# Optimization experiments

Hardware: AMD Instinct MI355X
Metric: run time of the kernel (lower is better)

## Reference

```python
import jax, jax.numpy as jnp
import numpy as np

B, S, D, H = 8, 1024, 1024, 16
DH = D // H  # 64


def setup_inputs() -> dict:
    key0 = jax.random.key(0)
    ks = jax.random.split(key0, 12)
    mk = lambda k, shape: jax.random.normal(k, shape, dtype=jnp.float32)
    inp = {
        "key": mk(ks[0], (B, S, D)),
        "value": mk(ks[1], (B, S, D)),
        "query": mk(ks[2], (B, S, D)),
        "mask": jax.random.randint(ks[3], (B, S, S), 0, 2).astype(jnp.bool_),
        "Wq": mk(ks[4], (D, D)) * 0.02, "bq": jnp.zeros((D,), jnp.float32),
        "Wk": mk(ks[5], (D, D)) * 0.02, "bk": jnp.zeros((D,), jnp.float32),
        "Wv": mk(ks[6], (D, D)) * 0.02, "bv": jnp.zeros((D,), jnp.float32),
        "Wo": mk(ks[7], (D, D)) * 0.02, "bo": jnp.zeros((D,), jnp.float32),
    }
    return inp


def _split_heads(x):
    # [B, S, D] -> [B, H, S, DH]
    return x.reshape(B, -1, H, DH).transpose(0, 2, 1, 3)


def reference(key, value, query, mask, Wq, bq, Wk, bk, Wv, bv, Wo, bo):
    # linear projections (nn.Linear: x @ W.T + b)
    q = _split_heads(query @ Wq.T + bq) / jnp.sqrt(jnp.float32(DH))
    k = _split_heads(key @ Wk.T + bk)
    v = _split_heads(value @ Wv.T + bv)
    # scores: [B, H, Q, K]
    scores = jnp.einsum("bhqd,bhkd->bhqk", q, k)
    scores = jnp.where(mask[:, None, :, :], jnp.float32(-1e18), scores)
    attn = jax.nn.softmax(scores, axis=-1)
    # dropout is identity in eval mode (deterministic reference)
    ctx = jnp.einsum("bhqk,bhkd->bhqd", attn, v)
    ctx = ctx.transpose(0, 2, 1, 3).reshape(B, -1, D)
    out = ctx @ Wo.T + bo
    return out, attn
```

## Files before the change

kernel.cpp:

```cpp
#include <hip/hip_runtime.h>
#include <hip/hip_bf16.h>

#define BB 8
#define SS 1024
#define DD 1024
#define HH 16
#define DHH 64
#define MM (BB*SS)

typedef __attribute__((ext_vector_type(8))) short short8;
typedef __attribute__((ext_vector_type(4))) float f32x4;
typedef __fp16 half2v __attribute__((ext_vector_type(2)));
typedef __fp16 half8 __attribute__((ext_vector_type(8)));

__device__ __forceinline__ unsigned short f2bf(float f) {
  union { __hip_bfloat16 b; unsigned short u; } cv;
  cv.b = __float2bfloat16(f);
  return cv.u;
}
__device__ __forceinline__ float bf2f(unsigned short u) {
  return __builtin_bit_cast(float, (unsigned)u << 16);
}

__global__ void k_conv_w(const float* __restrict__ in, unsigned short* __restrict__ out,
                         float scale, int n8) {
  int i = blockIdx.x * blockDim.x + threadIdx.x;
  if (i >= n8) return;
  const float4* in4 = (const float4*)in;
  float4 a = in4[i * 2];
  float4 b = in4[i * 2 + 1];
  unsigned int w[4];
  w[0] = f2bf(a.x * scale) | ((unsigned)f2bf(a.y * scale) << 16);
  w[1] = f2bf(a.z * scale) | ((unsigned)f2bf(a.w * scale) << 16);
  w[2] = f2bf(b.x * scale) | ((unsigned)f2bf(b.y * scale) << 16);
  w[3] = f2bf(b.z * scale) | ((unsigned)f2bf(b.w * scale) << 16);
  *(uint4*)(out + (size_t)i * 8) = *(uint4*)w;
}

__global__ void k_detect_mask(const unsigned int* __restrict__ m, int* __restrict__ flag) {
  if (threadIdx.x || blockIdx.x) return;
  int i32 = 1, f32m = 1;
  for (int i = 0; i < 64; ++i) {
    unsigned v = m[i];
    if (v > 1u) i32 = 0;
    if (v != 0u && v != 0x3F800000u) f32m = 0;
  }
  *flag = i32 ? 0 : (f32m ? 1 : 2);
}

__global__ void k_maskbits(const void* __restrict__ mask, const int* __restrict__ mmode,
                           unsigned short* __restrict__ out) {
  int i = blockIdx.x * blockDim.x + threadIdx.x;
  if (i >= BB * 32 * 64 * 32) return;
  int r = i & 31, cb = (i >> 5) & 63, qb = (i >> 11) & 31, b = i >> 16;
  size_t src = ((size_t)(b * SS + qb * 32 + r) * SS) + cb * 16;
  int mm = *mmode;
  unsigned short bits = 0;
  if (mm == 2) {
    const unsigned char* p = (const unsigned char*)mask + src;
    uint4 v = *(const uint4*)p;
    const unsigned char* bytes = (const unsigned char*)&v;
#pragma unroll
    for (int c = 0; c < 16; c++) bits |= (bytes[c] ? 1u : 0u) << c;
  } else {
    const unsigned int* p = (const unsigned int*)mask + src;
#pragma unroll
    for (int q = 0; q < 4; q++) {
      uint4 v = *(const uint4*)(p + q * 4);
      bits |= (v.x ? 1u : 0u) << (q * 4 + 0);
      bits |= (v.y ? 1u : 0u) << (q * 4 + 1);
      bits |= (v.z ? 1u : 0u) << (q * 4 + 2);
      bits |= (v.w ? 1u : 0u) << (q * 4 + 3);
    }
  }
  out[i] = bits;
}

__global__ void __launch_bounds__(256, 2) k_gemm_qkv(
    const float* __restrict__ Xq, const float* __restrict__ Xk, const float* __restrict__ Xv,
    const unsigned short* __restrict__ Wqb, const unsigned short* __restrict__ Wkb,
    const unsigned short* __restrict__ Wvb,
    const float* __restrict__ bq, const float* __restrict__ bk, const float* __restrict__ bv,
    unsigned short* __restrict__ Oq, unsigned short* __restrict__ Ok,
    unsigned short* __restrict__ Ov) {
  int z = blockIdx.z;
  const float* X = (z == 0) ? Xq : (z == 1 ? Xk : Xv);
  const unsigned short* W = (z == 0) ? Wqb : (z == 1 ? Wkb : Wvb);
  const float* bias = (z == 0) ? bq : (z == 1 ? bk : bv);
  float bsc = (z == 0) ? 0.125f : 1.0f;
  unsigned short* O = (z == 0) ? Oq : (z == 1 ? Ok : Ov);

  __shared__ alignas(16) unsigned char As[128 * 64 * 2];
  __shared__ alignas(16) unsigned char Bs[128 * 64 * 2];

  int t = threadIdx.x;
  int row0 = blockIdx.y * 128, col0 = blockIdx.x * 128;
  int w = t >> 6, lane = t & 63, lr = lane & 15, lg = lane >> 4;
  int wm = w >> 1, wn = w & 1;

  f32x4 z4 = {0.f, 0.f, 0.f, 0.f};
  f32x4 acc[4][4];
#pragma unroll
  for (int m = 0; m < 4; m++)
#pragma unroll
    for (int n = 0; n < 4; n++) acc[m][n] = z4;

  int ar = t >> 3, ac = t & 7;

  for (int kt = 0; kt < 16; ++kt) {
    int k0 = kt * 64;
#pragma unroll
    for (int p = 0; p < 4; ++p) {
      int r = p * 32 + ar;
      const float* src = X + (size_t)(row0 + r) * DD + k0 + ac * 8;
      float4 f0 = *(const float4*)src;
      float4 f1 = *(const float4*)(src + 4);
      unsigned int wb[4];
      wb[0] = f2bf(f0.x) | ((unsigned)f2bf(f0.y) << 16);
      wb[1] = f2bf(f0.z) | ((unsigned)f2bf(f0.w) << 16);
      wb[2] = f2bf(f1.x) | ((unsigned)f2bf(f1.y) << 16);
      wb[3] = f2bf(f1.z) | ((unsigned)f2bf(f1.w) << 16);
      int off = (r * 128 + ac * 16) ^ ((r & 7) << 4);
      *(uint4*)(As + off) = *(uint4*)wb;
    }
#pragma unroll
    for (int p = 0; p < 4; ++p) {
      int r = p * 32 + ar;
      uint4 v = *(const uint4*)(W + (size_t)(col0 + r) * DD + k0 + ac * 8);
      int off = (r * 128 + ac * 16) ^ ((r & 7) << 4);
      *(uint4*)(Bs + off) = v;
    }
    __syncthreads();
#pragma unroll
    for (int kk = 0; kk < 2; ++kk) {
      short8 af[4], bfr[4];
#pragma unroll
      for (int m = 0; m < 4; m++) {
        int r = wm * 64 + m * 16 + lr;
        af[m] = *(const short8*)(As + ((r * 128 + kk * 64 + lg * 16) ^ ((lr & 7) << 4)));
      }
#pragma unroll
      for (int n = 0; n < 4; n++) {
        int r = wn * 64 + n * 16 + lr;
        bfr[n] = *(const short8*)(Bs + ((r * 128 + kk * 64 + lg * 16) ^ ((lr & 7) << 4)));
      }
#pragma unroll
      for (int m = 0; m < 4; m++)
#pragma unroll
        for (int n = 0; n < 4; n++)
          acc[m][n] = __builtin_amdgcn_mfma_f32_16x16x32_bf16(af[m], bfr[n], acc[m][n], 0, 0, 0);
    }
    __syncthreads();
  }
#pragma unroll
  for (int m = 0; m < 4; m++) {
#pragma unroll
    for (int n = 0; n < 4; n++) {
      int col = col0 + wn * 64 + n * 16 + lr;
      float bv_ = bias[col] * bsc;
#pragma unroll
      for (int j = 0; j < 4; j++) {
        int row = row0 + wm * 64 + m * 16 + lg * 4 + j;
        O[(size_t)row * DD + col] = f2bf(acc[m][n][j] + bv_);
      }
    }
  }
}

__global__ void __launch_bounds__(256, 2) k_gemm_out(
    const unsigned short* __restrict__ A, const unsigned short* __restrict__ W,
    const float* __restrict__ bias, float* __restrict__ Out) {
  __shared__ alignas(16) unsigned char As[128 * 64 * 2];
  __shared__ alignas(16) unsigned char Bs[128 * 64 * 2];

  int t = threadIdx.x;
  int row0 = blockIdx.y * 128, col0 = blockIdx.x * 128;
  int w = t >> 6, lane = t & 63, lr = lane & 15, lg = lane >> 4;
  int wm = w >> 1, wn = w & 1;

  f32x4 z4 = {0.f, 0.f, 0.f, 0.f};
  f32x4 acc[4][4];
#pragma unroll
  for (int m = 0; m < 4; m++)
#pragma unroll
    for (int n = 0; n < 4; n++) acc[m][n] = z4;

  int ar = t >> 3, ac = t & 7;

  for (int kt = 0; kt < 16; ++kt) {
    int k0 = kt * 64;
#pragma unroll
    for (int p = 0; p < 4; ++p) {
      int r = p * 32 + ar;
      uint4 v = *(const uint4*)(A + (size_t)(row0 + r) * DD + k0 + ac * 8);
      int off = (r * 128 + ac * 16) ^ ((r & 7) << 4);
      *(uint4*)(As + off) = v;
    }
#pragma unroll
    for (int p = 0; p < 4; ++p) {
      int r = p * 32 + ar;
      uint4 v = *(const uint4*)(W + (size_t)(col0 + r) * DD + k0 + ac * 8);
      int off = (r * 128 + ac * 16) ^ ((r & 7) << 4);
      *(uint4*)(Bs + off) = v;
    }
    __syncthreads();
#pragma unroll
    for (int kk = 0; kk < 2; ++kk) {
      short8 af[4], bfr[4];
#pragma unroll
      for (int m = 0; m < 4; m++) {
        int r = wm * 64 + m * 16 + lr;
        af[m] = *(const short8*)(As + ((r * 128 + kk * 64 + lg * 16) ^ ((lr & 7) << 4)));
      }
#pragma unroll
      for (int n = 0; n < 4; n++) {
        int r = wn * 64 + n * 16 + lr;
        bfr[n] = *(const short8*)(Bs + ((r * 128 + kk * 64 + lg * 16) ^ ((lr & 7) << 4)));
      }
#pragma unroll
      for (int m = 0; m < 4; m++)
#pragma unroll
        for (int n = 0; n < 4; n++)
          acc[m][n] = __builtin_amdgcn_mfma_f32_16x16x32_bf16(af[m], bfr[n], acc[m][n], 0, 0, 0);
    }
    __syncthreads();
  }
#pragma unroll
  for (int m = 0; m < 4; m++) {
#pragma unroll
    for (int n = 0; n < 4; n++) {
      int col = col0 + wn * 64 + n * 16 + lr;
      float bv_ = bias[col];
#pragma unroll
      for (int j = 0; j < 4; j++) {
        int row = row0 + wm * 64 + m * 16 + lg * 4 + j;
        Out[(size_t)row * DD + col] = acc[m][n][j] + bv_;
      }
    }
  }
}

__global__ void k_transpose_v(const unsigned short* __restrict__ V,
                              unsigned short* __restrict__ VT) {
  int blk = blockIdx.x;
  int s0 = (blk & 15) * 64;
  int h = (blk >> 4) & 15;
  int b = blk >> 8;
  __shared__ alignas(16) unsigned short T[64][72];
  int t = threadIdx.x;
  int rr = t >> 3, cc = t & 7;
#pragma unroll
  for (int p = 0; p < 2; p++) {
    int r = p * 32 + rr;
    uint4 v = *(const uint4*)(V + (size_t)(b * SS + s0 + r) * DD + h * 64 + cc * 8);
    *(uint4*)(&T[r][cc * 8]) = v;
  }
  __syncthreads();
#pragma unroll
  for (int p = 0; p < 2; p++) {
    int dh = p * 32 + rr;
    unsigned short tmp[8];
#pragma unroll
    for (int i = 0; i < 8; i++) tmp[i] = T[cc * 8 + i][dh];
    unsigned outw[4];
#pragma unroll
    for (int i = 0; i < 4; i++) {
      half2v hp = __builtin_amdgcn_cvt_pkrtz(bf2f(tmp[2 * i]), bf2f(tmp[2 * i + 1]));
      outw[i] = __builtin_bit_cast(unsigned, hp);
    }
    *(uint4*)(VT + (size_t)((b * HH + h) * DHH + dh) * SS + s0 + cc * 8) = *(uint4*)outw;
  }
}

__global__ void __launch_bounds__(256) k_attn(
    const unsigned short* __restrict__ Q, const unsigned short* __restrict__ K,
    const unsigned short* __restrict__ VT, const unsigned short* __restrict__ mbits,
    float* __restrict__ attn, unsigned short* __restrict__ ctx) {
  int wg = blockIdx.x;
  int xcd = wg & 7, idx = wg >> 3;
  int p_bh = xcd + (idx >> 5) * 8;
  int qb = idx & 31;
  int b = p_bh >> 4, h = p_bh & 15;
  int q0 = qb * 32;
  int t = threadIdx.x, w = t >> 6, lane = t & 63, lr = lane & 15, lg = lane >> 4;

  __shared__ float redsum[4][32];
  __shared__ alignas(16) unsigned char pbuf[24576];
  unsigned short (*P)[32][72] = (unsigned short(*)[32][72])pbuf;
  float (*cred)[32][64] = (float(*)[32][64])pbuf;

  short8 qf[2][2];
#pragma unroll
  for (int m = 0; m < 2; m++)
#pragma unroll
    for (int kb = 0; kb < 2; kb++)
      qf[m][kb] = *(const short8*)(Q + (size_t)(b * SS + q0 + m * 16 + lr) * DD +
                                   h * 64 + kb * 32 + lg * 8);

  const unsigned short* mb = mbits + (size_t)(b * 32 + qb) * 64 * 32;

  f32x4 z4 = {0.f, 0.f, 0.f, 0.f};
  float ps[2][4];
#pragma unroll
  for (int m = 0; m < 2; m++)
#pragma unroll
    for (int j = 0; j < 4; j++) ps[m][j] = 0.f;

  half2v scp[2][16][2];
#pragma unroll
  for (int c = 0; c < 16; c++) {
    int colb = w * 256 + c * 16;
    const unsigned short* kp = K + (size_t)(b * SS + colb + lr) * DD + h * 64 + lg * 8;
    short8 kf0 = *(const short8*)kp;
    short8 kf1 = *(const short8*)(kp + 32);
    int cb = w * 16 + c;
#pragma unroll
    for (int m = 0; m < 2; m++) {
      f32x4 s = __builtin_amdgcn_mfma_f32_16x16x32_bf16(qf[m][0], kf0, z4, 0, 0, 0);
      s = __builtin_amdgcn_mfma_f32_16x16x32_bf16(qf[m][1], kf1, s, 0, 0, 0);
      const unsigned short* mrow = mb + cb * 32 + m * 16 + lg * 4;
      ushort4 mw = *(const ushort4*)mrow;
      unsigned short mwa[4] = {mw.x, mw.y, mw.z, mw.w};
      float p[4];
#pragma unroll
      for (int j = 0; j < 4; j++)
        p[j] = ((mwa[j] >> lr) & 1) ? 0.0f : __expf(fminf(s[j], 10.0f));
      half2v h0 = __builtin_amdgcn_cvt_pkrtz(p[0], p[1]);
      half2v h1 = __builtin_amdgcn_cvt_pkrtz(p[2], p[3]);
      scp[m][c][0] = h0;
      scp[m][c][1] = h1;
      ps[m][0] += (float)h0[0];
      ps[m][1] += (float)h0[1];
      ps[m][2] += (float)h1[0];
      ps[m][3] += (float)h1[1];
    }
  }
#pragma unroll
  for (int m = 0; m < 2; m++)
#pragma unroll
    for (int j = 0; j < 4; j++) {
      float v = ps[m][j];
      v += __shfl_xor(v, 1);
      v += __shfl_xor(v, 2);
      v += __shfl_xor(v, 4);
      v += __shfl_xor(v, 8);
      ps[m][j] = v;
    }
  if (lr == 0) {
#pragma unroll
    for (int m = 0; m < 2; m++)
#pragma unroll
      for (int j = 0; j < 4; j++) redsum[w][m * 16 + lg * 4 + j] = ps[m][j];
  }
  __syncthreads();
  float inv[2][4];
#pragma unroll
  for (int m = 0; m < 2; m++)
#pragma unroll
    for (int j = 0; j < 4; j++) {
      int r = m * 16 + lg * 4 + j;
      inv[m][j] = 1.f / (redsum[0][r] + redsum[1][r] + redsum[2][r] + redsum[3][r]);
    }
  float invr[4];
#pragma unroll
  for (int rg = 0; rg < 4; rg++) {
    int r = rg * 8 + (lane >> 3);
    invr[rg] = 1.f / (redsum[0][r] + redsum[1][r] + redsum[2][r] + redsum[3][r]);
  }

  float* ab = attn + (size_t)((b * HH + h) * SS + q0) * SS;
  f32x4 cacc[2][4];
#pragma unroll
  for (int m = 0; m < 2; m++)
#pragma unroll
    for (int nb = 0; nb < 4; nb++) cacc[m][nb] = z4;

#pragma unroll
  for (int ch = 0; ch < 4; ch++) {
#pragma unroll
    for (int cc = 0; cc < 4; cc++) {
      int c = ch * 4 + cc;
      int col = cc * 16 + lr;
#pragma unroll
      for (int m = 0; m < 2; m++) {
        unsigned u0 = __builtin_bit_cast(unsigned, scp[m][c][0]);
        unsigned u1 = __builtin_bit_cast(unsigned, scp[m][c][1]);
        int r0 = m * 16 + lg * 4;
        P[w][r0 + 0][col] = (unsigned short)(u0 & 0xffffu);
        P[w][r0 + 1][col] = (unsigned short)(u0 >> 16);
        P[w][r0 + 2][col] = (unsigned short)(u1 & 0xffffu);
        P[w][r0 + 3][col] = (unsigned short)(u1 >> 16);
      }
    }
#pragma unroll
    for (int rg = 0; rg < 4; rg++) {
      int row = rg * 8 + (lane >> 3);
      float iv = invr[rg];
#pragma unroll
      for (int ci = 0; ci < 2; ci++) {
        int col = (lane & 7) * 4 + ci * 32;
        ushort4 hv = *(const ushort4*)(&P[w][row][col]);
        f32x4 o;
        o[0] = (float)__builtin_bit_cast(__fp16, hv.x) * iv;
        o[1] = (float)__builtin_bit_cast(__fp16, hv.y) * iv;
        o[2] = (float)__builtin_bit_cast(__fp16, hv.z) * iv;
        o[3] = (float)__builtin_bit_cast(__fp16, hv.w) * iv;
        __builtin_nontemporal_store(o, (f32x4*)(ab + (size_t)row * SS + w * 256 + ch * 64 + col));
      }
    }
#pragma unroll
    for (int kb = 0; kb < 2; kb++) {
      half8 vf[4];
#pragma unroll
      for (int nb = 0; nb < 4; nb++)
        vf[nb] = __builtin_bit_cast(half8,
            *(const short8*)(VT + (size_t)((b * HH + h) * DHH + nb * 16 + lr) * SS +
                             w * 256 + ch * 64 + kb * 32 + lg * 8));
      half8 pa[2];
#pragma unroll
      for (int m = 0; m < 2; m++)
        pa[m] = __builtin_bit_cast(half8, *(const short8*)(&P[w][m * 16 + lr][kb * 32 + lg * 8]));
#pragma unroll
      for (int m = 0; m < 2; m++)
#pragma unroll
        for (int nb = 0; nb < 4; nb++)
          cacc[m][nb] = __builtin_amdgcn_mfma_f32_16x16x32_f16(pa[m], vf[nb], cacc[m][nb], 0, 0, 0);
    }
  }
  __syncthreads();
  if (w > 0) {
#pragma unroll
    for (int m = 0; m < 2; m++)
#pragma unroll
      for (int nb = 0; nb < 4; nb++)
#pragma unroll
        for (int j = 0; j < 4; j++)
          cred[w - 1][m * 16 + lg * 4 + j][nb * 16 + lr] = cacc[m][nb][j];
  }
  __syncthreads();
  if (w == 0) {
#pragma unroll
    for (int m = 0; m < 2; m++)
#pragma unroll
      for (int nb = 0; nb < 4; nb++) {
        int col = nb * 16 + lr;
#pragma unroll
        for (int j = 0; j < 4; j++) {
          int rl = m * 16 + lg * 4 + j;
          float v = (cacc[m][nb][j] + cred[0][rl][col] + cred[1][rl][col] + cred[2][rl][col]) *
                    inv[m][j];
          ctx[(size_t)(b * SS + q0 + rl) * DD + h * 64 + col] = f2bf(v);
        }
      }
  }
}

extern "C" void kernel_launch(void* const* d_in, const int* in_sizes, int n_in,
                              void* d_out, int out_size, void* d_ws, size_t ws_size,
                              hipStream_t stream) {
  const float* key   = (const float*)d_in[0];
  const float* value = (const float*)d_in[1];
  const float* query = (const float*)d_in[2];
  const void*  mask  = d_in[3];
  const float* Wq = (const float*)d_in[4];
  const float* bq = (const float*)d_in[5];
  const float* Wk = (const float*)d_in[6];
  const float* bk = (const float*)d_in[7];
  const float* Wv = (const float*)d_in[8];
  const float* bv = (const float*)d_in[9];
  const float* Wo = (const float*)d_in[10];
  const float* bo = (const float*)d_in[11];

  unsigned short* wq_b = (unsigned short*)d_ws;
  unsigned short* wk_b = wq_b + (size_t)DD * DD;
  unsigned short* wv_b = wk_b + (size_t)DD * DD;
  unsigned short* wo_b = wv_b + (size_t)DD * DD;
  unsigned short* Qb   = wo_b + (size_t)DD * DD;
  unsigned short* Kb   = Qb + (size_t)MM * DD;
  unsigned short* Vb   = Kb + (size_t)MM * DD;
  unsigned short* VTb  = Vb + (size_t)MM * DD;
  unsigned short* CTXb = VTb + (size_t)MM * DD;
  unsigned short* MB   = CTXb + (size_t)MM * DD;
  int* flag = (int*)(MB + (size_t)BB * 32 * 64 * 32);
  size_t needed = (size_t)(4 * DD * DD + 5 * MM * DD) * 2 + (1u << 20) + 256;
  if (ws_size < needed) return;

  float* out  = (float*)d_out;
  float* attn = out + (size_t)MM * DD;

  k_conv_w<<<512, 256, 0, stream>>>(Wq, wq_b, 0.125f, DD * DD / 8);
  k_conv_w<<<512, 256, 0, stream>>>(Wk, wk_b, 1.0f, DD * DD / 8);
  k_conv_w<<<512, 256, 0, stream>>>(Wv, wv_b, 1.0f, DD * DD / 8);
  k_conv_w<<<512, 256, 0, stream>>>(Wo, wo_b, 1.0f, DD * DD / 8);
  k_detect_mask<<<1, 1, 0, stream>>>((const unsigned int*)mask, flag);
  k_maskbits<<<2048, 256, 0, stream>>>(mask, flag, MB);
  k_gemm_qkv<<<dim3(8, 64, 3), 256, 0, stream>>>(query, key, value, wq_b, wk_b, wv_b,
                                                 bq, bk, bv, Qb, Kb, Vb);
  k_transpose_v<<<2048, 256, 0, stream>>>(Vb, VTb);
  k_attn<<<4096, 256, 0, stream>>>(Qb, Kb, VTb, MB, attn, CTXb);
  k_gemm_out<<<dim3(8, 64, 1), 256, 0, stream>>>(CTXb, wo_b, bo, out);
}
```

Baseline: 396.6 us.

## Pre-convert activations to bf16 and stage GEMM tiles with direct global-to-LDS loads

Adds three elementwise conversion launches that turn the fp32 query/key/value inputs into bf16 copies, using the not-yet-written attention output buffer as scratch. The QKV projection then reads bf16 like the output GEMM does. Both GEMMs now use global_load_lds with 16-byte transfers to fill shared-memory tiles directly, skipping the VGPR staging and the in-loop fp32-to-bf16 packing. The trade-offs are extra full passes over the activations for conversion, and loss of the XOR swizzle on the LDS tiles, which may cause bank conflicts on the fragment reads.

```diff
diff --git a/kernel.cpp b/kernel.cpp
--- a/kernel.cpp
+++ b/kernel.cpp
@@ -12,6 +12,9 @@
 typedef __attribute__((ext_vector_type(4))) float f32x4;
 typedef __fp16 half2v __attribute__((ext_vector_type(2)));
 typedef __fp16 half8 __attribute__((ext_vector_type(8)));
+
+typedef __attribute__((address_space(3))) void lds_void;
+typedef const __attribute__((address_space(1))) void gbl_void;
 
 __device__ __forceinline__ unsigned short f2bf(float f) {
   union { __hip_bfloat16 b; unsigned short u; } cv;
@@ -77,14 +80,15 @@
 }
 
 __global__ void __launch_bounds__(256, 2) k_gemm_qkv(
-    const float* __restrict__ Xq, const float* __restrict__ Xk, const float* __restrict__ Xv,
+    const unsigned short* __restrict__ Xq, const unsigned short* __restrict__ Xk,
+    const unsigned short* __restrict__ Xv,
     const unsigned short* __restrict__ Wqb, const unsigned short* __restrict__ Wkb,
     const unsigned short* __restrict__ Wvb,
     const float* __restrict__ bq, const float* __restrict__ bk, const float* __restrict__ bv,
     unsigned short* __restrict__ Oq, unsigned short* __restrict__ Ok,
     unsigned short* __restrict__ Ov) {
   int z = blockIdx.z;
-  const float* X = (z == 0) ? Xq : (z == 1 ? Xk : Xv);
+  const unsigned short* A = (z == 0) ? Xq : (z == 1 ? Xk : Xv);
   const unsigned short* W = (z == 0) ? Wqb : (z == 1 ? Wkb : Wvb);
   const float* bias = (z == 0) ? bq : (z == 1 ? bk : bv);
   float bsc = (z == 0) ? 0.125f : 1.0f;
@@ -98,6 +102,9 @@
   int w = t >> 6, lane = t & 63, lr = lane & 15, lg = lane >> 4;
   int wm = w >> 1, wn = w & 1;
 
+  int srow = w * 8 + (lane >> 3);
+  int scol = (lane & 7) * 8;
+
   f32x4 z4 = {0.f, 0.f, 0.f, 0.f};
   f32x4 acc[4][4];
 #pragma unroll
@@ -105,30 +112,17 @@
 #pragma unroll
     for (int n = 0; n < 4; n++) acc[m][n] = z4;
 
-  int ar = t >> 3, ac = t & 7;
-
   for (int kt = 0; kt < 16; ++kt) {
     int k0 = kt * 64;
 #pragma unroll
-    for (int p = 0; p < 4; ++p) {
-      int r = p * 32 + ar;
-      const float* src = X + (size_t)(row0 + r) * DD + k0 + ac * 8;
-      float4 f0 = *(const float4*)src;
-      float4 f1 = *(const float4*)(src + 4);
-      unsigned int wb[4];
-      wb[0] = f2bf(f0.x) | ((unsigned)f2bf(f0.y) << 16);
-      wb[1] = f2bf(f0.z) | ((unsigned)f2bf(f0.w) << 16);
-      wb[2] = f2bf(f1.x) | ((unsigned)f2bf(f1.y) << 16);
-      wb[3] = f2bf(f1.z) | ((unsigned)f2bf(f1.w) << 16);
-      int off = (r * 128 + ac * 16) ^ ((r & 7) << 4);
-      *(uint4*)(As + off) = *(uint4*)wb;
-    }
-#pragma unroll
-    for (int p = 0; p < 4; ++p) {
-      int r = p * 32 + ar;
-      uint4 v = *(const uint4*)(W + (size_t)(col0 + r) * DD + k0 + ac * 8);
-      int off = (r * 128 + ac * 16) ^ ((r & 7) << 4);
-      *(uint4*)(Bs + off) = v;
+    for (int i = 0; i < 4; ++i) {
+      int r = i * 32 + srow;
+      __builtin_amdgcn_global_load_lds(
+          (gbl_void*)(A + (size_t)(row0 + r) * DD + k0 + scol),
+          (lds_void*)(As + (i * 32 + w * 8) * 128), 16, 0, 0);
+      __builtin_amdgcn_global_load_lds(
+          (gbl_void*)(W + (size_t)(col0 + r) * DD + k0 + scol),
+          (lds_void*)(Bs + (i * 32 + w * 8) * 128), 16, 0, 0);
     }
     __syncthreads();
 #pragma unroll
@@ -137,12 +131,12 @@
 #pragma unroll
       for (int m = 0; m < 4; m++) {
         int r = wm * 64 + m * 16 + lr;
-        af[m] = *(const short8*)(As + ((r * 128 + kk * 64 + lg * 16) ^ ((lr & 7) << 4)));
+        af[m] = *(const short8*)(As + r * 128 + kk * 64 + lg * 16);
       }
 #pragma unroll
       for (int n = 0; n < 4; n++) {
         int r = wn * 64 + n * 16 + lr;
-        bfr[n] = *(const short8*)(Bs + ((r * 128 + kk * 64 + lg * 16) ^ ((lr & 7) << 4)));
+        bfr[n] = *(const short8*)(Bs + r * 128 + kk * 64 + lg * 16);
       }
 #pragma unroll
       for (int m = 0; m < 4; m++)
@@ -178,6 +172,9 @@
   int w = t >> 6, lane = t & 63, lr = lane & 15, lg = lane >> 4;
   int wm = w >> 1, wn = w & 1;
 
+  int srow = w * 8 + (lane >> 3);
+  int scol = (lane & 7) * 8;
+
   f32x4 z4 = {0.f, 0.f, 0.f, 0.f};
   f32x4 acc[4][4];
 #pragma unroll
@@ -185,23 +182,17 @@
 #pragma unroll
     for (int n = 0; n < 4; n++) acc[m][n] = z4;
 
-  int ar = t >> 3, ac = t & 7;
-
   for (int kt = 0; kt < 16; ++kt) {
     int k0 = kt * 64;
 #pragma unroll
-    for (int p = 0; p < 4; ++p) {
-      int r = p * 32 + ar;
-      uint4 v = *(const uint4*)(A + (size_t)(row0 + r) * DD + k0 + ac * 8);
-      int off = (r * 128 + ac * 16) ^ ((r & 7) << 4);
-      *(uint4*)(As + off) = v;
-    }
-#pragma unroll
-    for (int p = 0; p < 4; ++p) {
-      int r = p * 32 + ar;
-      uint4 v = *(const uint4*)(W + (size_t)(col0 + r) * DD + k0 + ac * 8);
-      int off = (r * 128 + ac * 16) ^ ((r & 7) << 4);
-      *(uint4*)(Bs + off) = v;
+    for (int i = 0; i < 4; ++i) {
+      int r = i * 32 + srow;
+      __builtin_amdgcn_global_load_lds(
+          (gbl_void*)(A + (size_t)(row0 + r) * DD + k0 + scol),
+          (lds_void*)(As + (i * 32 + w * 8) * 128), 16, 0, 0);
+      __builtin_amdgcn_global_load_lds(
+          (gbl_void*)(W + (size_t)(col0 + r) * DD + k0 + scol),
+          (lds_void*)(Bs + (i * 32 + w * 8) * 128), 16, 0, 0);
     }
     __syncthreads();
 #pragma unroll
@@ -210,12 +201,12 @@
 #pragma unroll
       for (int m = 0; m < 4; m++) {
         int r = wm * 64 + m * 16 + lr;
-        af[m] = *(const short8*)(As + ((r * 128 + kk * 64 + lg * 16) ^ ((lr & 7) << 4)));
+        af[m] = *(const short8*)(As + r * 128 + kk * 64 + lg * 16);
       }
 #pragma unroll
       for (int n = 0; n < 4; n++) {
         int r = wn * 64 + n * 16 + lr;
-        bfr[n] = *(const short8*)(Bs + ((r * 128 + kk * 64 + lg * 16) ^ ((lr & 7) << 4)));
+        bfr[n] = *(const short8*)(Bs + r * 128 + kk * 64 + lg * 16);
       }
 #pragma unroll
       for (int m = 0; m < 4; m++)
@@ -488,13 +479,20 @@
   float* out  = (float*)d_out;
   float* attn = out + (size_t)MM * DD;
 
+  unsigned short* Xq_b = (unsigned short*)attn;
+  unsigned short* Xk_b = Xq_b + (size_t)MM * DD;
+  unsigned short* Xv_b = Xk_b + (size_t)MM * DD;
+
   k_conv_w<<<512, 256, 0, stream>>>(Wq, wq_b, 0.125f, DD * DD / 8);
   k_conv_w<<<512, 256, 0, stream>>>(Wk, wk_b, 1.0f, DD * DD / 8);
   k_conv_w<<<512, 256, 0, stream>>>(Wv, wv_b, 1.0f, DD * DD / 8);
   k_conv_w<<<512, 256, 0, stream>>>(Wo, wo_b, 1.0f, DD * DD / 8);
+  k_conv_w<<<4096, 256, 0, stream>>>(query, Xq_b, 1.0f, MM * DD / 8);
+  k_conv_w<<<4096, 256, 0, stream>>>(key,   Xk_b, 1.0f, MM * DD / 8);
+  k_conv_w<<<4096, 256, 0, stream>>>(value, Xv_b, 1.0f, MM * DD / 8);
   k_detect_mask<<<1, 1, 0, stream>>>((const unsigned int*)mask, flag);
   k_maskbits<<<2048, 256, 0, stream>>>(mask, flag, MB);
-  k_gemm_qkv<<<dim3(8, 64, 3), 256, 0, stream>>>(query, key, value, wq_b, wk_b, wv_b,
+  k_gemm_qkv<<<dim3(8, 64, 3), 256, 0, stream>>>(Xq_b, Xk_b, Xv_b, wq_b, wk_b, wv_b,
                                                  bq, bk, bv, Qb, Kb, Vb);
   k_transpose_v<<<2048, 256, 0, stream>>>(Vb, VTb);
   k_attn<<<4096, 256, 0, stream>>>(Qb, Kb, VTb, MB, attn, CTXb);
```

Result: faster. 341.9 us (-13.8%).
